# Performance work log

Measured on AMD Instinct MI355X. Metric: run time of the kernel, lower is better.

## Reference

```python
import jax, jax.numpy as jnp
import numpy as np

EPS = 1e-6
B, H, S, D = 8, 16, 4096, 64


def setup_inputs() -> dict:
    key = jax.random.key(0)
    k1, k2, k3 = jax.random.split(key, 3)
    return {
        "keys": jax.random.normal(k1, (B, H, S, D), dtype=jnp.float32),
        "values": jax.random.normal(k2, (B, H, S, D), dtype=jnp.float32),
        "queries": jax.random.normal(k3, (B, H, S, D), dtype=jnp.float32),
    }


def reference(keys, values, queries):
    # update: accumulate outer-product associative memory per (batch, head)
    # M[b,h] = sum_s k_s outer v_s  -> [B, H, D, D]
    M = jnp.einsum("bhsd,bhse->bhde", keys, values)
    # normalizer z[b,h] = sum_s k_s -> [B, H, D]
    z = jnp.sum(keys, axis=2)
    # retrieve: out = (q @ M) / (q . z + eps)
    num = jnp.einsum("bhqd,bhde->bhqe", queries, M)        # [B, H, S, D]
    den = jnp.einsum("bhqd,bhd->bhq", queries, z) + EPS     # [B, H, S]
    return num / den[..., None]
```

## Files before the change

### kernel.cpp

```cpp
#include <hip/hip_runtime.h>

constexpr int Sc = 4096, Dc = 64;
constexpr int BH = 128;
constexpr int SS = 8;
constexpr int CHUNK = Sc / SS;
constexpr int SROWS = 32;
constexpr int NST = CHUNK / SROWS;
constexpr int MM = Dc * Dc;
constexpr int NZP = SS * 4;
constexpr int QT = 128;

using sh8 = __attribute__((ext_vector_type(8))) short;
using f32x4 = __attribute__((ext_vector_type(4))) float;

__device__ __forceinline__ unsigned int packbf2(float lo, float hi) {
  unsigned int a = __builtin_bit_cast(unsigned int, lo);
  unsigned int b = __builtin_bit_cast(unsigned int, hi);
  a = (a + 0x7fffu + ((a >> 16) & 1u)) >> 16;
  b = (b + 0x7fffu + ((b >> 16) & 1u)) & 0xffff0000u;
  return a | b;
}

__global__ __launch_bounds__(256) void k1_accum(const float* __restrict__ K,
                                                const float* __restrict__ V,
                                                float* __restrict__ Pm,
                                                double* __restrict__ Pz) {
  const int blk = blockIdx.x, bh = blk >> 3, ck = blk & 7;
  const int tid = threadIdx.x, w = tid >> 6, l = tid & 63;
  const int g = l >> 4, c = l & 15;

  const size_t base = ((size_t)bh * Sc + (size_t)ck * CHUNK) * Dc;
  const float* kcol = K + base + 16 * w + c;
  const float* vcol = V + base + c;

  f32x4 acc[4];
  #pragma unroll
  for (int i = 0; i < 4; ++i) acc[i] = (f32x4){0.f, 0.f, 0.f, 0.f};
  double zacc = 0.0;

  for (int st = 0; st < NST; ++st) {
    const int rowf = (st * SROWS + 8 * g) * Dc;

    float ak[8];
    #pragma unroll
    for (int j = 0; j < 8; ++j) ak[j] = kcol[rowf + j * Dc];

    float bv[4][8];
    #pragma unroll
    for (int et = 0; et < 4; ++et)
      #pragma unroll
      for (int j = 0; j < 8; ++j) bv[et][j] = vcol[rowf + j * Dc + 16 * et];

    #pragma unroll
    for (int j = 0; j < 8; ++j) zacc += (double)ak[j];

    unsigned int au[4];
    #pragma unroll
    for (int j = 0; j < 4; ++j) au[j] = packbf2(ak[2 * j], ak[2 * j + 1]);
    const sh8 afr = __builtin_bit_cast(sh8, *(const uint4*)au);

    #pragma unroll
    for (int et = 0; et < 4; ++et) {
      unsigned int bu[4];
      #pragma unroll
      for (int j = 0; j < 4; ++j) bu[j] = packbf2(bv[et][2 * j], bv[et][2 * j + 1]);
      const sh8 bfr = __builtin_bit_cast(sh8, *(const uint4*)bu);
      acc[et] = __builtin_amdgcn_mfma_f32_16x16x32_bf16(afr, bfr, acc[et], 0, 0, 0);
    }
  }

  float* pd = Pm + ((size_t)ck * BH + bh) * MM;
  #pragma unroll
  for (int et = 0; et < 4; ++et)
    #pragma unroll
    for (int r = 0; r < 4; ++r)
      pd[(16 * w + 4 * g + r) * 64 + 16 * et + c] = acc[et][r];

  Pz[((size_t)(ck * 4 + g) * BH + bh) * Dc + 16 * w + c] = zacc;
}

__global__ __launch_bounds__(256) void k2_reduce(const float* __restrict__ Pm,
                                                 const double* __restrict__ Pz,
                                                 float* __restrict__ Fm,
                                                 float* __restrict__ Fz) {
  const int i = blockIdx.x * 256 + threadIdx.x;
  const int nm = BH * MM;
  if (i < nm) {
    float s = 0.f;
    #pragma unroll
    for (int cc = 0; cc < SS; ++cc) s += Pm[(size_t)cc * nm + i];
    Fm[i] = s;
  }
  const int nz = BH * Dc;
  if (i < nz) {
    double s = 0.0;
    #pragma unroll
    for (int cc = 0; cc < NZP; ++cc) s += Pz[(size_t)cc * nz + i];
    Fz[i] = (float)s;
  }
}

__global__ __launch_bounds__(256) void k3_retrieve(const float* __restrict__ Q,
                                                   const float* __restrict__ Fm,
                                                   const float* __restrict__ Fz,
                                                   float* __restrict__ O) {
  const int blk = blockIdx.x;
  const int bh = blk >> 5;
  const int row0 = (blk & 31) * QT;

  __shared__ __align__(16) float lm[Dc][Dc];
  __shared__ __align__(16) float lq[QT][68];
  __shared__ __align__(16) float lz[Dc];

  const int tid = threadIdx.x;

  const float4* gm4 = (const float4*)(Fm + (size_t)bh * MM);
  float4* lm4 = (float4*)&lm[0][0];
  #pragma unroll
  for (int j = 0; j < 4; ++j) lm4[tid + j * 256] = gm4[tid + j * 256];
  if (tid < Dc) lz[tid] = Fz[(size_t)bh * Dc + tid];

  const float4* gq4 = (const float4*)(Q + ((size_t)bh * Sc + row0) * Dc);
  #pragma unroll
  for (int j = 0; j < 8; ++j) {
    const int i4 = tid + j * 256;
    const float4 v = gq4[i4];
    const int f = i4 * 4;
    *(float4*)&lq[f >> 6][f & 63] = v;
  }
  __syncthreads();

  const int rg = tid >> 3;
  const int cg = tid & 7;
  const int r0 = rg * 4;
  const int e0 = cg * 8;

  float acc[4][8] = {};
  double den[4] = {0.0, 0.0, 0.0, 0.0};

  #pragma unroll
  for (int ds = 0; ds < 16; ++ds) {
    const int d0 = ds * 4;
    const float4 z4 = *(const float4*)&lz[d0];
    const float* zf = (const float*)&z4;
    float4 q4[4];
    #pragma unroll
    for (int r = 0; r < 4; ++r) q4[r] = *(const float4*)&lq[r0 + r][d0];
    const float* qf[4] = {(const float*)&q4[0], (const float*)&q4[1],
                          (const float*)&q4[2], (const float*)&q4[3]};
    #pragma unroll
    for (int i = 0; i < 4; ++i) {
      const float4 ma = *(const float4*)&lm[d0 + i][e0];
      const float4 mb = *(const float4*)&lm[d0 + i][e0 + 4];
      const float mf[8] = {ma.x, ma.y, ma.z, ma.w, mb.x, mb.y, mb.z, mb.w};
      const double zd = (double)zf[i];
      #pragma unroll
      for (int r = 0; r < 4; ++r) {
        const float qs = qf[r][i];
        den[r] += (double)qs * zd;
        #pragma unroll
        for (int j = 0; j < 8; ++j)
          acc[r][j] = fmaf(qs, mf[j], acc[r][j]);
      }
    }
  }

  #pragma unroll
  for (int r = 0; r < 4; ++r) {
    const double iv = 1.0 / (den[r] + 1e-6);
    float* go = O + ((size_t)bh * Sc + row0 + r0 + r) * Dc + e0;
    ((float4*)go)[0] = make_float4((float)((double)acc[r][0] * iv),
                                   (float)((double)acc[r][1] * iv),
                                   (float)((double)acc[r][2] * iv),
                                   (float)((double)acc[r][3] * iv));
    ((float4*)go)[1] = make_float4((float)((double)acc[r][4] * iv),
                                   (float)((double)acc[r][5] * iv),
                                   (float)((double)acc[r][6] * iv),
                                   (float)((double)acc[r][7] * iv));
  }
}

extern "C" void kernel_launch(void* const* d_in, const int* in_sizes, int n_in,
                              void* d_out, int out_size, void* d_ws, size_t ws_size,
                              hipStream_t stream) {
  const float* K = (const float*)d_in[0];
  const float* V = (const float*)d_in[1];
  const float* Q = (const float*)d_in[2];
  float* O = (float*)d_out;

  float* Pm = (float*)d_ws;
  float* Fm = Pm + (size_t)SS * BH * MM;
  double* Pz = (double*)(Fm + (size_t)BH * MM);
  float* Fz = (float*)(Pz + (size_t)NZP * BH * Dc);

  hipLaunchKernelGGL(k1_accum, dim3(BH * SS), dim3(256), 0, stream, K, V, Pm, Pz);
  hipLaunchKernelGGL(k2_reduce, dim3((BH * MM + 255) / 256), dim3(256), 0, stream, Pm, Pz, Fm, Fz);
  hipLaunchKernelGGL(k3_retrieve, dim3(BH * (Sc / QT)), dim3(256), 0, stream, Q, Fm, Fz, O);
}
```

Baseline: 169.0 us.

## Double-buffer K/V tiles in LDS via async global_load_lds in accumulate kernel

```diff
diff --git a/kernel.cpp b/kernel.cpp
--- a/kernel.cpp
+++ b/kernel.cpp
@@ -12,6 +12,8 @@
 
 using sh8 = __attribute__((ext_vector_type(8))) short;
 using f32x4 = __attribute__((ext_vector_type(4))) float;
+typedef __attribute__((address_space(1))) const unsigned int as1_u32;
+typedef __attribute__((address_space(3))) unsigned int as3_u32;
 
 __device__ __forceinline__ unsigned int packbf2(float lo, float hi) {
   unsigned int a = __builtin_bit_cast(unsigned int, lo);
@@ -30,30 +32,48 @@
   const int g = l >> 4, c = l & 15;
 
   const size_t base = ((size_t)bh * Sc + (size_t)ck * CHUNK) * Dc;
-  const float* kcol = K + base + 16 * w + c;
-  const float* vcol = V + base + c;
+  const float* Kg = K + base;
+  const float* Vg = V + base;
+
+  __shared__ __align__(16) float smem[2 * 4096];
+
+  const int lofs = w * 512 + l * 4;
 
   f32x4 acc[4];
   #pragma unroll
   for (int i = 0; i < 4; ++i) acc[i] = (f32x4){0.f, 0.f, 0.f, 0.f};
   double zacc = 0.0;
 
-  for (int st = 0; st < NST; ++st) {
-    const int rowf = (st * SROWS + 8 * g) * Dc;
+#define K1_ISSUE(T, BUF)                                                         \
+  {                                                                              \
+    const float* gk_ = Kg + (size_t)(T) * 2048 + lofs;                           \
+    const float* gv_ = Vg + (size_t)(T) * 2048 + lofs;                           \
+    float* lk_ = &smem[(BUF) * 4096 + w * 512];           \
+    float* lv_ = &smem[(BUF) * 4096 + 2048 + w * 512];                           \
+    __builtin_amdgcn_global_load_lds((as1_u32*)gk_,         (as3_u32*)lk_,         16, 0, 0); \
+    __builtin_amdgcn_global_load_lds((as1_u32*)(gk_ + 256), (as3_u32*)(lk_ + 256), 16, 0, 0); \
+    __builtin_amdgcn_global_load_lds((as1_u32*)gv_,         (as3_u32*)lv_,         16, 0, 0); \
+    __builtin_amdgcn_global_load_lds((as1_u32*)(gv_ + 256), (as3_u32*)(lv_ + 256), 16, 0, 0); \
+  }
+
+  K1_ISSUE(0, 0)
+
+  for (int t = 0; t < NST; ++t) {
+    const int buf = t & 1;
+    asm volatile("s_waitcnt vmcnt(0)" ::: "memory");
+    asm volatile("s_waitcnt lgkmcnt(0)" ::: "memory");
+    __builtin_amdgcn_s_barrier();
+    if (t + 1 < NST) K1_ISSUE(t + 1, buf ^ 1)
+
+    const float* bK = &smem[buf * 4096];
+    const float* bV = &smem[buf * 4096 + 2048];
+
+    #pragma unroll
+    for (int r = 0; r < 8; ++r) zacc += (double)bK[(8 * w + r) * 64 + l];
 
     float ak[8];
     #pragma unroll
-    for (int j = 0; j < 8; ++j) ak[j] = kcol[rowf + j * Dc];
-
-    float bv[4][8];
-    #pragma unroll
-    for (int et = 0; et < 4; ++et)
-      #pragma unroll
-      for (int j = 0; j < 8; ++j) bv[et][j] = vcol[rowf + j * Dc + 16 * et];
-
-    #pragma unroll
-    for (int j = 0; j < 8; ++j) zacc += (double)ak[j];
-
+    for (int j = 0; j < 8; ++j) ak[j] = bK[(8 * g + j) * 64 + 16 * w + c];
     unsigned int au[4];
     #pragma unroll
     for (int j = 0; j < 4; ++j) au[j] = packbf2(ak[2 * j], ak[2 * j + 1]);
@@ -61,13 +81,17 @@
 
     #pragma unroll
     for (int et = 0; et < 4; ++et) {
+      float bv[8];
+      #pragma unroll
+      for (int j = 0; j < 8; ++j) bv[j] = bV[(8 * g + j) * 64 + 16 * et + c];
       unsigned int bu[4];
       #pragma unroll
-      for (int j = 0; j < 4; ++j) bu[j] = packbf2(bv[et][2 * j], bv[et][2 * j + 1]);
+      for (int j = 0; j < 4; ++j) bu[j] = packbf2(bv[2 * j], bv[2 * j + 1]);
       const sh8 bfr = __builtin_bit_cast(sh8, *(const uint4*)bu);
       acc[et] = __builtin_amdgcn_mfma_f32_16x16x32_bf16(afr, bfr, acc[et], 0, 0, 0);
     }
   }
+#undef K1_ISSUE
 
   float* pd = Pm + ((size_t)ck * BH + bh) * MM;
   #pragma unroll
@@ -76,7 +100,7 @@
     for (int r = 0; r < 4; ++r)
       pd[(16 * w + 4 * g + r) * 64 + 16 * et + c] = acc[et][r];
 
-  Pz[((size_t)(ck * 4 + g) * BH + bh) * Dc + 16 * w + c] = zacc;
+  Pz[((size_t)(ck * 4 + w) * BH + bh) * Dc + l] = zacc;
 }
 
 __global__ __launch_bounds__(256) void k2_reduce(const float* __restrict__ Pm,
```

After: 162.8 us. 3.7% less time.
